# Optimization experiments

Hardware: AMD Instinct MI355X
Metric: run time of the kernel (lower is better)

Reference implementation:

```python
import jax, jax.numpy as jnp
import numpy as np

D = 768
H = 12
HD = D // H
HID = 3072
EPS = 1e-5


def layer_norm(x, g, b):
    m = jnp.mean(x, axis=-1, keepdims=True)
    v = jnp.mean((x - m) ** 2, axis=-1, keepdims=True)
    return (x - m) * jax.lax.rsqrt(v + EPS) * g + b


def setup_inputs() -> dict:
    key = jax.random.key(0)
    ks = jax.random.split(key, 8)
    s_in = 1.0 / np.sqrt(D)
    s_hid = 1.0 / np.sqrt(HID)
    return {
        "x": jax.random.normal(ks[0], (32, 577, D), dtype=jnp.float32),
        "w_qkv": jax.random.normal(ks[1], (D, 3 * D), dtype=jnp.float32) * s_in,
        "b_qkv": jnp.zeros((3 * D,), dtype=jnp.float32),
        "w_proj": jax.random.normal(ks[2], (D, D), dtype=jnp.float32) * s_in,
        "b_proj": jnp.zeros((D,), dtype=jnp.float32),
        "g1": jnp.ones((D,), jnp.float32), "be1": jnp.zeros((D,), jnp.float32),
        "g2": jnp.ones((D,), jnp.float32), "be2": jnp.zeros((D,), jnp.float32),
        "g3": jnp.ones((D,), jnp.float32), "be3": jnp.zeros((D,), jnp.float32),
        "w1": jax.random.normal(ks[3], (D, HID), dtype=jnp.float32) * s_in,
        "bm1": jnp.zeros((HID,), dtype=jnp.float32),
        "w2": jax.random.normal(ks[4], (HID, D), dtype=jnp.float32) * s_hid,
        "bm2": jnp.zeros((D,), dtype=jnp.float32),
    }


def reference(x, w_qkv, b_qkv, w_proj, b_proj, g1, be1, g2, be2, g3, be3, w1, bm1, w2, bm2):
    B, N, _ = x.shape
    scale = 1.0 / np.sqrt(HD).astype(np.float32)

    # --- attention block ---
    h = layer_norm(x, g1, be1)
    qkv = h @ w_qkv + b_qkv                       # [B,N,3D]
    q, k, v = jnp.split(qkv, 3, axis=-1)
    q = q.reshape(B, N, H, HD).transpose(0, 2, 1, 3)  # [B,H,N,hd]
    k = k.reshape(B, N, H, HD).transpose(0, 2, 1, 3)
    v = v.reshape(B, N, H, HD).transpose(0, 2, 1, 3)
    scores = jnp.einsum("bhnd,bhmd->bhnm", q, k) * scale  # materialized O(N^2), as in source
    probs = jax.nn.softmax(scores, axis=-1)
    attn = jnp.einsum("bhnm,bhmd->bhnd", probs, v)
    attn = attn.transpose(0, 2, 1, 3).reshape(B, N, D)
    attn = attn @ w_proj + b_proj
    res1 = x + attn

    # --- MLP block (note: source applies LayerNorm2 AND the MLP's own LayerNorm) ---
    h = layer_norm(res1, g2, be2)
    h = layer_norm(h, g3, be3)
    h = jax.nn.gelu(h @ w1 + bm1, approximate=False)
    h = h @ w2 + bm2  # dropout = identity at eval
    return res1 + h
```

## Files before the change

kernel.cpp:

```cpp
#include <hip/hip_runtime.h>
#include <hip/hip_bf16.h>


#define M_ROWS 18464
#define NHEAD 12

typedef __attribute__((ext_vector_type(8))) short s16x8;
typedef __attribute__((ext_vector_type(4))) float f32x4;

__device__ __forceinline__ unsigned short f2bf(float f) {
  union { float f; unsigned u; } v; v.f = f;
  return (unsigned short)((v.u + 0x7fffu + ((v.u >> 16) & 1u)) >> 16);
}
__device__ __forceinline__ float bf2f(unsigned short h) {
  union { unsigned u; float f; } v; v.u = ((unsigned)h) << 16;
  return v.f;
}

__device__ __forceinline__ void gload_lds16(const void* g, void* l) {
  __builtin_amdgcn_global_load_lds((const __attribute__((address_space(1))) unsigned*)g,
                                   (__attribute__((address_space(3))) unsigned*)l, 16, 0, 0);
}

__global__ __launch_bounds__(256) void wtrans(const float* __restrict__ in,
                                              unsigned short* __restrict__ out,
                                              int K, int N) {
  __shared__ float t[32][33];
  const int n0 = blockIdx.x * 32, k0 = blockIdx.y * 32;
  const int tx = threadIdx.x, ty = threadIdx.y;
  for (int i = ty; i < 32; i += 8)
    t[i][tx] = in[(size_t)(k0 + i) * N + n0 + tx];
  __syncthreads();
  for (int i = ty; i < 32; i += 8)
    out[(size_t)(n0 + i) * K + k0 + tx] = f2bf(t[tx][i]);
}

__global__ __launch_bounds__(256) void ln1_kernel(const float* __restrict__ x,
    const float* __restrict__ g, const float* __restrict__ be,
    unsigned short* __restrict__ out) {
  const int w = threadIdx.x >> 6, l = threadIdx.x & 63;
  const size_t row = (size_t)blockIdx.x * 4 + w;
  const float* xr = x + row * 768;
  f32x4 v[3];
#pragma unroll
  for (int s = 0; s < 3; s++) v[s] = ((const f32x4*)xr)[s * 64 + l];
  float sm = 0.f, sq = 0.f;
#pragma unroll
  for (int s = 0; s < 3; s++)
#pragma unroll
    for (int j = 0; j < 4; j++) { sm += v[s][j]; sq += v[s][j] * v[s][j]; }
#pragma unroll
  for (int o = 1; o < 64; o <<= 1) { sm += __shfl_xor(sm, o); sq += __shfl_xor(sq, o); }
  const float mean = sm * (1.f / 768.f);
  const float rs = rsqrtf(sq * (1.f / 768.f) - mean * mean + 1e-5f);
  unsigned short* orow = out + row * 768;
#pragma unroll
  for (int s = 0; s < 3; s++) {
    int col = s * 256 + l * 4;
    unsigned short h4[4];
#pragma unroll
    for (int j = 0; j < 4; j++)
      h4[j] = f2bf((v[s][j] - mean) * rs * g[col + j] + be[col + j]);
    uint2 u; u.x = h4[0] | ((unsigned)h4[1] << 16); u.y = h4[2] | ((unsigned)h4[3] << 16);
    *(uint2*)(orow + col) = u;
  }
}

__global__ __launch_bounds__(256) void ln2_kernel(const float* __restrict__ xin,
    const float* __restrict__ g2, const float* __restrict__ be2,
    const float* __restrict__ g3, const float* __restrict__ be3,
    unsigned short* __restrict__ out) {
  const int w = threadIdx.x >> 6, l = threadIdx.x & 63;
  const size_t row = (size_t)blockIdx.x * 4 + w;
  const float* xr = xin + row * 768;
  f32x4 v[3];
#pragma unroll
  for (int s = 0; s < 3; s++) v[s] = ((const f32x4*)xr)[s * 64 + l];
  float sm = 0.f, sq = 0.f;
#pragma unroll
  for (int s = 0; s < 3; s++)
#pragma unroll
    for (int j = 0; j < 4; j++) { sm += v[s][j]; sq += v[s][j] * v[s][j]; }
#pragma unroll
  for (int o = 1; o < 64; o <<= 1) { sm += __shfl_xor(sm, o); sq += __shfl_xor(sq, o); }
  float mean = sm * (1.f / 768.f);
  float rs = rsqrtf(sq * (1.f / 768.f) - mean * mean + 1e-5f);
  float y[12];
  sm = 0.f; sq = 0.f;
#pragma unroll
  for (int s = 0; s < 3; s++) {
    int col = s * 256 + l * 4;
#pragma unroll
    for (int j = 0; j < 4; j++) {
      float t = (v[s][j] - mean) * rs * g2[col + j] + be2[col + j];
      y[s * 4 + j] = t; sm += t; sq += t * t;
    }
  }
#pragma unroll
  for (int o = 1; o < 64; o <<= 1) { sm += __shfl_xor(sm, o); sq += __shfl_xor(sq, o); }
  mean = sm * (1.f / 768.f);
  rs = rsqrtf(sq * (1.f / 768.f) - mean * mean + 1e-5f);
  unsigned short* orow = out + row * 768;
#pragma unroll
  for (int s = 0; s < 3; s++) {
    int col = s * 256 + l * 4;
    unsigned short h4[4];
#pragma unroll
    for (int j = 0; j < 4; j++)
      h4[j] = f2bf((y[s * 4 + j] - mean) * rs * g3[col + j] + be3[col + j]);
    uint2 u; u.x = h4[0] | ((unsigned)h4[1] << 16); u.y = h4[2] | ((unsigned)h4[3] << 16);
    *(uint2*)(orow + col) = u;
  }
}

template<int EPI>
__global__ __launch_bounds__(256) void gemm_nt(
    const unsigned short* __restrict__ A, const unsigned short* __restrict__ BT,
    const float* __restrict__ bias, const float* __restrict__ aux,
    void* __restrict__ Cout, int M, int N, int K) {
  __shared__ unsigned short As[128 * 32];
  __shared__ unsigned short Bs[128 * 32];
  const int tid = threadIdx.x;
  const int w = tid >> 6, l = tid & 63;
  const int m0 = blockIdx.y * 128, n0 = blockIdx.x * 128;
  const int r0 = w * 32 + (l >> 2);
  const int kof = (l & 3) * 8;
  const int lr = l & 15, lg = l >> 4;
  const int wr = (w >> 1) * 64, wc = (w & 1) * 64;
  f32x4 acc[4][4];
#pragma unroll
  for (int m = 0; m < 4; m++)
#pragma unroll
    for (int n = 0; n < 4; n++)
#pragma unroll
      for (int r = 0; r < 4; r++) acc[m][n][r] = 0.f;

  char* AsB = (char*)As; char* BsB = (char*)Bs;
  int ar0 = m0 + r0;      if (ar0 >= M) ar0 = M - 1;
  int ar1 = m0 + r0 + 16; if (ar1 >= M) ar1 = M - 1;
  const size_t a0 = (size_t)ar0 * K + kof;
  const size_t a1 = (size_t)ar1 * K + kof;
  const size_t b0 = (size_t)(n0 + r0) * K + kof;
  const size_t b1 = (size_t)(n0 + r0 + 16) * K + kof;

  for (int k0 = 0; k0 < K; k0 += 32) {
    __syncthreads();
    gload_lds16(A + a0 + k0, AsB + (w * 2 + 0) * 1024);
    gload_lds16(A + a1 + k0, AsB + (w * 2 + 1) * 1024);
    gload_lds16(BT + b0 + k0, BsB + (w * 2 + 0) * 1024);
    gload_lds16(BT + b1 + k0, BsB + (w * 2 + 1) * 1024);
    __syncthreads();
    s16x8 af[4], bf[4];
#pragma unroll
    for (int m = 0; m < 4; m++)
      af[m] = *(const s16x8*)(AsB + (wr + m * 16 + lr) * 64 + lg * 16);
#pragma unroll
    for (int n = 0; n < 4; n++)
      bf[n] = *(const s16x8*)(BsB + (wc + n * 16 + lr) * 64 + lg * 16);
#pragma unroll
    for (int m = 0; m < 4; m++)
#pragma unroll
      for (int n = 0; n < 4; n++)
        acc[m][n] = __builtin_amdgcn_mfma_f32_16x16x32_bf16(af[m], bf[n], acc[m][n], 0, 0, 0);
  }

  float bs[4];
#pragma unroll
  for (int n = 0; n < 4; n++) bs[n] = bias[n0 + wc + n * 16 + lr];
#pragma unroll
  for (int m = 0; m < 4; m++) {
#pragma unroll
    for (int r = 0; r < 4; r++) {
      int row = m0 + wr + m * 16 + lg * 4 + r;
      if (row >= M) continue;
      size_t rb = (size_t)row * N;
#pragma unroll
      for (int n = 0; n < 4; n++) {
        int col = n0 + wc + n * 16 + lr;
        float c = acc[m][n][r] + bs[n];
        if (EPI == 0) {
          ((unsigned short*)Cout)[rb + col] = f2bf(c);
        } else if (EPI == 1) {
          ((float*)Cout)[rb + col] = c + aux[rb + col];
        } else if (EPI == 2) {
          c = 0.5f * c * (1.f + erff(c * 0.70710678118f));
          ((unsigned short*)Cout)[rb + col] = f2bf(c);
        } else {
          ((float*)Cout)[rb + col] = c + aux[rb + col];
        }
      }
    }
  }
}

__global__ __launch_bounds__(256) void attn_kernel(const unsigned short* __restrict__ qkv,
                                                   unsigned short* __restrict__ out) {
  __shared__ unsigned short Pl[4 * 16 * 72];
  __shared__ unsigned short VT[64 * 72];
  const int tid = threadIdx.x;
  const int w = tid >> 6, l = tid & 63;
  const int lr = l & 15, lg = l >> 4;
  const int bh = blockIdx.x / 10, qt = blockIdx.x % 10;
  const int b = bh / NHEAD, h = bh % NHEAD;
  const size_t base = (size_t)b * 577 * 2304 + (size_t)h * 64;
  int qr = qt * 64 + w * 16 + lr; int qrc = qr > 576 ? 576 : qr;
  const unsigned short* qp = qkv + base + (size_t)qrc * 2304;
  const s16x8 qf0 = *(const s16x8*)(qp + lg * 8);
  const s16x8 qf1 = *(const s16x8*)(qp + 32 + lg * 8);
  f32x4 oacc[4];
#pragma unroll
  for (int d = 0; d < 4; d++)
#pragma unroll
    for (int r = 0; r < 4; r++) oacc[d][r] = 0.f;
  float mrun = -3e38f, lrun = 0.f;
  unsigned short* Pw = Pl + w * 16 * 72;

  for (int kt = 0; kt < 10; kt++) {
    __syncthreads();
#pragma unroll
    for (int c = 0; c < 2; c++) {
      int cid = c * 256 + tid;
      int kc = cid >> 3, d0 = (cid & 7) * 8;
      int vr = kt * 64 + kc; if (vr > 576) vr = 576;
      s16x8 vv = *(const s16x8*)(qkv + base + 1536 + (size_t)vr * 2304 + d0);
#pragma unroll
      for (int j = 0; j < 8; j++)
        VT[(d0 + j) * 72 + kc] = (unsigned short)vv[j];
    }
    float sv[16];
#pragma unroll
    for (int sub = 0; sub < 4; sub++) {
      int kc = kt * 64 + sub * 16 + lr; if (kc > 576) kc = 576;
      const unsigned short* kp = qkv + base + 768 + (size_t)kc * 2304;
      s16x8 kf0 = *(const s16x8*)(kp + lg * 8);
      s16x8 kf1 = *(const s16x8*)(kp + 32 + lg * 8);
      f32x4 st;
#pragma unroll
      for (int r = 0; r < 4; r++) st[r] = 0.f;
      st = __builtin_amdgcn_mfma_f32_16x16x32_bf16(kf0, qf0, st, 0, 0, 0);
      st = __builtin_amdgcn_mfma_f32_16x16x32_bf16(kf1, qf1, st, 0, 0, 0);
#pragma unroll
      for (int r = 0; r < 4; r++) {
        int kcg = kt * 64 + sub * 16 + lg * 4 + r;
        sv[sub * 4 + r] = (kcg <= 576) ? st[r] * 0.125f : -3e38f;
      }
    }
    float tm = sv[0];
#pragma unroll
    for (int i = 1; i < 16; i++) tm = fmaxf(tm, sv[i]);
    tm = fmaxf(tm, __shfl_xor(tm, 16));
    tm = fmaxf(tm, __shfl_xor(tm, 32));
    float mnew = fmaxf(mrun, tm);
    float fac = __expf(mrun - mnew);
    mrun = mnew;
    float ts = 0.f;
    unsigned short pb[16];
#pragma unroll
    for (int i = 0; i < 16; i++) {
      float p = __expf(sv[i] - mnew);
      ts += p;
      pb[i] = f2bf(p);
    }
    ts += __shfl_xor(ts, 16);
    ts += __shfl_xor(ts, 32);
    lrun = lrun * fac + ts;
#pragma unroll
    for (int sub = 0; sub < 4; sub++) {
      uint2 u;
      u.x = (unsigned)pb[sub * 4 + 0] | ((unsigned)pb[sub * 4 + 1] << 16);
      u.y = (unsigned)pb[sub * 4 + 2] | ((unsigned)pb[sub * 4 + 3] << 16);
      *(uint2*)(Pw + lr * 72 + sub * 16 + lg * 4) = u;
    }
    float fr[4];
#pragma unroll
    for (int r = 0; r < 4; r++) fr[r] = __shfl(fac, lg * 4 + r);
#pragma unroll
    for (int d = 0; d < 4; d++)
#pragma unroll
      for (int r = 0; r < 4; r++) oacc[d][r] *= fr[r];
    __syncthreads();
#pragma unroll
    for (int hf = 0; hf < 2; hf++) {
      s16x8 pf = *(const s16x8*)(Pw + lr * 72 + hf * 32 + lg * 8);
#pragma unroll
      for (int d = 0; d < 4; d++) {
        s16x8 vf = *(const s16x8*)(VT + (d * 16 + lr) * 72 + hf * 32 + lg * 8);
        oacc[d] = __builtin_amdgcn_mfma_f32_16x16x32_bf16(pf, vf, oacc[d], 0, 0, 0);
      }
    }
  }
#pragma unroll
  for (int r = 0; r < 4; r++) {
    int qg = qt * 64 + w * 16 + lg * 4 + r;
    if (qg > 576) continue;
    float inv = 1.f / __shfl(lrun, lg * 4 + r);
#pragma unroll
    for (int d = 0; d < 4; d++)
      out[(size_t)(b * 577 + qg) * 768 + h * 64 + d * 16 + lr] = f2bf(oacc[d][r] * inv);
  }
}

extern "C" void kernel_launch(void* const* d_in, const int* in_sizes, int n_in,
                              void* d_out, int out_size, void* d_ws, size_t ws_size,
                              hipStream_t stream) {
  const float* x      = (const float*)d_in[0];
  const float* w_qkv  = (const float*)d_in[1];
  const float* b_qkv  = (const float*)d_in[2];
  const float* w_proj = (const float*)d_in[3];
  const float* b_proj = (const float*)d_in[4];
  const float* g1  = (const float*)d_in[5];
  const float* be1 = (const float*)d_in[6];
  const float* g2  = (const float*)d_in[7];
  const float* be2 = (const float*)d_in[8];
  const float* g3  = (const float*)d_in[9];
  const float* be3 = (const float*)d_in[10];
  const float* w1  = (const float*)d_in[11];
  const float* bm1 = (const float*)d_in[12];
  const float* w2  = (const float*)d_in[13];
  const float* bm2 = (const float*)d_in[14];

  char* ws = (char*)d_ws;
  unsigned short* wqkvT  = (unsigned short*)(ws + 0);
  unsigned short* wprojT = (unsigned short*)(ws + 3538944);
  unsigned short* w1T    = (unsigned short*)(ws + 4718592);
  unsigned short* w2T    = (unsigned short*)(ws + 9437184);
  unsigned short* hbuf   = (unsigned short*)(ws + 14155776);
  unsigned short* qkv    = (unsigned short*)(ws + 42516480);
  unsigned short* hid    = qkv;
  unsigned short* attnb  = hbuf;
  float*          res1   = (float*)(ws + 155959296);

  dim3 b32(32, 8);
  wtrans<<<dim3(2304 / 32, 768 / 32),  b32, 0, stream>>>(w_qkv,  wqkvT,  768, 2304);
  wtrans<<<dim3(768 / 32, 768 / 32),   b32, 0, stream>>>(w_proj, wprojT, 768, 768);
  wtrans<<<dim3(3072 / 32, 768 / 32),  b32, 0, stream>>>(w1,     w1T,    768, 3072);
  wtrans<<<dim3(768 / 32, 3072 / 32),  b32, 0, stream>>>(w2,     w2T,    3072, 768);

  ln1_kernel<<<4616, 256, 0, stream>>>(x, g1, be1, hbuf);
  gemm_nt<0><<<dim3(18, 145), 256, 0, stream>>>(hbuf, wqkvT, b_qkv, nullptr, qkv, M_ROWS, 2304, 768);
  attn_kernel<<<3840, 256, 0, stream>>>(qkv, attnb);
  gemm_nt<1><<<dim3(6, 145), 256, 0, stream>>>(attnb, wprojT, b_proj, x, res1, M_ROWS, 768, 768);
  ln2_kernel<<<4616, 256, 0, stream>>>(res1, g2, be2, g3, be3, hbuf);
  gemm_nt<2><<<dim3(24, 145), 256, 0, stream>>>(hbuf, w1T, bm1, nullptr, hid, M_ROWS, 3072, 768);
  gemm_nt<3><<<dim3(6, 145), 256, 0, stream>>>(hid, w2T, bm2, res1, (float*)d_out, M_ROWS, 768, 3072);
}
```

Baseline: 848.5 us.

## Double-buffer GEMM LDS tiles and remap workgroups across XCDs

The GEMM now keeps two LDS buffers for the A and B tiles. It issues the global-to-LDS loads for the next K step before running the MFMAs on the current one, which drops one barrier per iteration and overlaps memory latency with compute. It also remaps workgroup IDs so that consecutive tiles land on the same XCD, aiming for better L2 reuse. This doubles LDS use, which may cut occupancy. Because the async LDS loads rely on a single barrier, correctness depends on the wait behaviour around __syncthreads.

```diff
diff --git a/kernel.cpp b/kernel.cpp
--- a/kernel.cpp
+++ b/kernel.cpp
@@ -118,24 +118,30 @@
     const unsigned short* __restrict__ A, const unsigned short* __restrict__ BT,
     const float* __restrict__ bias, const float* __restrict__ aux,
     void* __restrict__ Cout, int M, int N, int K) {
-  __shared__ unsigned short As[128 * 32];
-  __shared__ unsigned short Bs[128 * 32];
+  __shared__ unsigned short As[2][128 * 32];
+  __shared__ unsigned short Bs[2][128 * 32];
   const int tid = threadIdx.x;
   const int w = tid >> 6, l = tid & 63;
-  const int m0 = blockIdx.y * 128, n0 = blockIdx.x * 128;
+  const int gx = (int)gridDim.x;
+  const int nwg = gx * (int)gridDim.y;
+  const int orig = (int)blockIdx.y * gx + (int)blockIdx.x;
+  const int q = nwg >> 3, r = nwg & 7, xcd = orig & 7, slot = orig >> 3;
+  const int newid = (xcd < r ? xcd * (q + 1) : r * (q + 1) + (xcd - r) * q) + slot;
+  const int m0 = (newid / gx) * 128, n0 = (newid % gx) * 128;
+
   const int r0 = w * 32 + (l >> 2);
   const int kof = (l & 3) * 8;
   const int lr = l & 15, lg = l >> 4;
   const int wr = (w >> 1) * 64, wc = (w & 1) * 64;
+  const int woff = w * 2048;
   f32x4 acc[4][4];
 #pragma unroll
   for (int m = 0; m < 4; m++)
 #pragma unroll
     for (int n = 0; n < 4; n++)
 #pragma unroll
-      for (int r = 0; r < 4; r++) acc[m][n][r] = 0.f;
-
-  char* AsB = (char*)As; char* BsB = (char*)Bs;
+      for (int r4 = 0; r4 < 4; r4++) acc[m][n][r4] = 0.f;
+
   int ar0 = m0 + r0;      if (ar0 >= M) ar0 = M - 1;
   int ar1 = m0 + r0 + 16; if (ar1 >= M) ar1 = M - 1;
   const size_t a0 = (size_t)ar0 * K + kof;
@@ -143,13 +149,23 @@
   const size_t b0 = (size_t)(n0 + r0) * K + kof;
   const size_t b1 = (size_t)(n0 + r0 + 16) * K + kof;
 
+  gload_lds16(A + a0, (char*)As[0] + woff);
+  gload_lds16(A + a1, (char*)As[0] + woff + 1024);
+  gload_lds16(BT + b0, (char*)Bs[0] + woff);
+  gload_lds16(BT + b1, (char*)Bs[0] + woff + 1024);
+  __syncthreads();
+
+  int cur = 0;
   for (int k0 = 0; k0 < K; k0 += 32) {
-    __syncthreads();
-    gload_lds16(A + a0 + k0, AsB + (w * 2 + 0) * 1024);
-    gload_lds16(A + a1 + k0, AsB + (w * 2 + 1) * 1024);
-    gload_lds16(BT + b0 + k0, BsB + (w * 2 + 0) * 1024);
-    gload_lds16(BT + b1 + k0, BsB + (w * 2 + 1) * 1024);
-    __syncthreads();
+    const int kn = k0 + 32;
+    if (kn < K) {
+      gload_lds16(A + a0 + kn, (char*)As[cur ^ 1] + woff);
+      gload_lds16(A + a1 + kn, (char*)As[cur ^ 1] + woff + 1024);
+      gload_lds16(BT + b0 + kn, (char*)Bs[cur ^ 1] + woff);
+      gload_lds16(BT + b1 + kn, (char*)Bs[cur ^ 1] + woff + 1024);
+    }
+    const char* AsB = (const char*)As[cur];
+    const char* BsB = (const char*)Bs[cur];
     s16x8 af[4], bf[4];
 #pragma unroll
     for (int m = 0; m < 4; m++)
@@ -162,6 +178,8 @@
 #pragma unroll
       for (int n = 0; n < 4; n++)
         acc[m][n] = __builtin_amdgcn_mfma_f32_16x16x32_bf16(af[m], bf[n], acc[m][n], 0, 0, 0);
+    __syncthreads();
+    cur ^= 1;
   }
 
   float bs[4];
@@ -170,14 +188,14 @@
 #pragma unroll
   for (int m = 0; m < 4; m++) {
 #pragma unroll
-    for (int r = 0; r < 4; r++) {
-      int row = m0 + wr + m * 16 + lg * 4 + r;
+    for (int r4 = 0; r4 < 4; r4++) {
+      int row = m0 + wr + m * 16 + lg * 4 + r4;
       if (row >= M) continue;
       size_t rb = (size_t)row * N;
 #pragma unroll
       for (int n = 0; n < 4; n++) {
         int col = n0 + wc + n * 16 + lr;
-        float c = acc[m][n][r] + bs[n];
+        float c = acc[m][n][r4] + bs[n];
         if (EPI == 0) {
           ((unsigned short*)Cout)[rb + col] = f2bf(c);
         } else if (EPI == 1) {
```

Result: faster. 819.9 us (-3.4%).
